# Kernel optimization log

Hardware: AMD Instinct MI355X
Metric: run time of the kernel (lower is better)

The kernel has to match this reference:

```python
import jax, jax.numpy as jnp
import numpy as np

N_NODES = 100000
N_EDGES = 1600000
C_IN = 128
C_OUT = 128


def setup_inputs() -> dict:
    key = jax.random.key(0)
    k1, k2, k3, k4 = jax.random.split(key, 4)
    x = jax.random.normal(k1, (N_NODES, C_IN), dtype=jnp.float32)
    edge_index = jax.random.randint(k2, (2, N_EDGES), 0, N_NODES, dtype=jnp.int64)
    W = jax.random.normal(k3, (C_IN, C_OUT), dtype=jnp.float32) * (1.0 / np.sqrt(C_IN))
    b = jax.random.normal(k4, (C_OUT,), dtype=jnp.float32) * 0.01
    return {"x": x, "edge_index": edge_index, "W": W, "b": b}


def reference(x, edge_index, W, b):
    # EffSparseEdgeOnlyConv with aggr='add':
    #   x2  = lin2(x)
    #   deg = A @ ones         (per-destination-node edge count)
    #   out = A @ x2 - x2 * deg
    n = x.shape[0]
    dst = edge_index[0]  # COO row indices (aggregation target)
    src = edge_index[1]  # COO col indices (message source)
    x2 = x @ W + b  # [N, C_out]
    deg = jax.ops.segment_sum(
        jnp.ones((src.shape[0],), dtype=x.dtype), dst, num_segments=n
    )[:, None]  # [N, 1]
    agg = jax.ops.segment_sum(x2[src], dst, num_segments=n)  # [N, C_out]
    return agg - x2 * deg
```

## Files before the change

kernel.cpp:

```cpp
#include <hip/hip_runtime.h>


#define C_DIM 128
#define EPB 8192
#define MAXBK 1024

typedef __attribute__((ext_vector_type(8))) short bf16x8;
typedef __attribute__((ext_vector_type(4))) float f32x4;

__device__ __forceinline__ ushort f2b(float f) {
    uint u = __float_as_uint(f);
    u = (u + 0x7FFFu + ((u >> 16) & 1u)) >> 16;
    return (ushort)u;
}
__device__ __forceinline__ float b2f_lo(uint u) { return __uint_as_float(u << 16); }
__device__ __forceinline__ float b2f_hi(uint u) { return __uint_as_float(u & 0xFFFF0000u); }

__global__ __launch_bounds__(256) void gemm_mfma(const float* __restrict__ x,
                                                 const float* __restrict__ W,
                                                 float* __restrict__ x2f,
                                                 ushort* __restrict__ x2b,
                                                 int nrows) {
    __shared__ ushort Wt[128 * 128];
    const int tid = threadIdx.x;
    for (int i = tid; i < 4096; i += 256) {
        int k = i >> 5, n0 = (i & 31) * 4;
        float4 w = *(const float4*)(W + k * 128 + n0);
        float wv[4] = {w.x, w.y, w.z, w.w};
#pragma unroll
        for (int j = 0; j < 4; j++) {
            int n = n0 + j;
            Wt[(n * 128 + k) ^ ((n & 7) << 3)] = f2b(wv[j]);
        }
    }
    __syncthreads();

    const int wv_ = tid >> 6;
    const int lane = tid & 63;
    const int ln = lane & 15, kg = lane >> 4;
    const int row_base = blockIdx.x * 128 + wv_ * 32;

    f32x4 acc[2][8];
#pragma unroll
    for (int a = 0; a < 2; a++)
#pragma unroll
        for (int b = 0; b < 8; b++) acc[a][b] = (f32x4)(0.f);

#pragma unroll
    for (int step = 0; step < 4; step++) {
        const int k0 = step * 32 + kg * 8;
        bf16x8 bfr[8];
#pragma unroll
        for (int cf = 0; cf < 8; cf++) {
            int n = cf * 16 + ln;
            bfr[cf] = *(const bf16x8*)&Wt[(n * 128 + k0) ^ ((n & 7) << 3)];
        }
#pragma unroll
        for (int mf = 0; mf < 2; mf++) {
            int row = row_base + mf * 16 + ln;
            bf16x8 afr;
#pragma unroll
            for (int j = 0; j < 8; j++) afr[j] = 0;
            if (row < nrows) {
                const float4* ap = (const float4*)(x + (size_t)row * 128 + k0);
                float4 a0 = ap[0], a1 = ap[1];
                float av[8] = {a0.x, a0.y, a0.z, a0.w, a1.x, a1.y, a1.z, a1.w};
#pragma unroll
                for (int j = 0; j < 8; j++) afr[j] = (short)f2b(av[j]);
            }
#pragma unroll
            for (int cf = 0; cf < 8; cf++)
                acc[mf][cf] = __builtin_amdgcn_mfma_f32_16x16x32_bf16(afr, bfr[cf], acc[mf][cf], 0, 0, 0);
        }
    }

#pragma unroll
    for (int mf = 0; mf < 2; mf++) {
#pragma unroll
        for (int j = 0; j < 4; j++) {
            int row = row_base + mf * 16 + kg * 4 + j;
            if (row >= nrows) continue;
#pragma unroll
            for (int cf = 0; cf < 8; cf++) {
                float v = acc[mf][cf][j];
                int col = cf * 16 + ln;
                x2f[(size_t)row * 128 + col] = v;
                if (x2b) x2b[(size_t)row * 128 + col] = f2b(v);
            }
        }
    }
}

__global__ __launch_bounds__(256) void zero_ints(int* p, int n) {
    int i = blockIdx.x * 256 + threadIdx.x;
    if (i < n) p[i] = 0;
}

__global__ __launch_bounds__(256) void count_deg(const int* __restrict__ ei,
                                                 int* __restrict__ cnt, int ne, int nn) {
    int e = blockIdx.x * 256 + threadIdx.x;
    if (e >= ne) return;
    int dst = ei[e];
    if ((unsigned)dst < (unsigned)nn) atomicAdd(&cnt[dst], 1);
}

__global__ __launch_bounds__(256) void scan_partials(const int* __restrict__ cnt,
                                                     int* __restrict__ bsum, int n) {
    __shared__ int red[256];
    int i = blockIdx.x * 1024 + threadIdx.x * 4;
    int s = 0;
    if (i + 3 < n) {
        int4 v = *(const int4*)(cnt + i);
        s = v.x + v.y + v.z + v.w;
    } else {
        for (int j = i; j < n && j < i + 4; j++) s += cnt[j];
    }
    red[threadIdx.x] = s;
    __syncthreads();
    for (int off = 128; off > 0; off >>= 1) {
        if (threadIdx.x < off) red[threadIdx.x] += red[threadIdx.x + off];
        __syncthreads();
    }
    if (threadIdx.x == 0) bsum[blockIdx.x] = red[0];
}

__global__ __launch_bounds__(1024) void scan_bsums(int* __restrict__ bsum, int nb) {
    __shared__ int s[1024];
    int v = (threadIdx.x < nb) ? bsum[threadIdx.x] : 0;
    s[threadIdx.x] = v;
    __syncthreads();
    for (int off = 1; off < 1024; off <<= 1) {
        int t = (threadIdx.x >= off) ? s[threadIdx.x - off] : 0;
        __syncthreads();
        s[threadIdx.x] += t;
        __syncthreads();
    }
    if (threadIdx.x < nb) bsum[threadIdx.x] = s[threadIdx.x] - v;
}

__global__ __launch_bounds__(256) void scan_apply(const int* __restrict__ cnt,
                                                  const int* __restrict__ bsum,
                                                  int* __restrict__ start, int n) {
    __shared__ int s[256];
    int i = blockIdx.x * 1024 + threadIdx.x * 4;
    int4 v = make_int4(0, 0, 0, 0);
    if (i + 3 < n) {
        v = *(const int4*)(cnt + i);
    } else {
        if (i + 0 < n) v.x = cnt[i + 0];
        if (i + 1 < n) v.y = cnt[i + 1];
        if (i + 2 < n) v.z = cnt[i + 2];
        if (i + 3 < n) v.w = cnt[i + 3];
    }
    int tsum = v.x + v.y + v.z + v.w;
    s[threadIdx.x] = tsum;
    __syncthreads();
    for (int off = 1; off < 256; off <<= 1) {
        int t = (threadIdx.x >= off) ? s[threadIdx.x - off] : 0;
        __syncthreads();
        s[threadIdx.x] += t;
        __syncthreads();
    }
    int r0 = s[threadIdx.x] - tsum + bsum[blockIdx.x];
    int r1 = r0 + v.x, r2 = r1 + v.y, r3 = r2 + v.z;
    if (i + 3 < n) {
        *(int4*)(start + i) = make_int4(r0, r1, r2, r3);
    } else {
        int rr[4] = {r0, r1, r2, r3};
        for (int j = 0; j < 4 && i + j < n; j++) start[i + j] = rr[j];
    }
}

__global__ __launch_bounds__(256) void bin_edges2(const int* __restrict__ ei,
                                                  const int* __restrict__ start,
                                                  int* __restrict__ bnext,
                                                  uint* __restrict__ bbuf,
                                                  int ne, int nn, int nbk) {
    __shared__ int hist[MAXBK];
    __shared__ int base[MAXBK];
    const int e0 = blockIdx.x * EPB;
    const int e1 = min(ne, e0 + EPB);
    for (int i = threadIdx.x; i < nbk; i += 256) hist[i] = 0;
    __syncthreads();
    for (int e = e0 + threadIdx.x; e < e1; e += 256) {
        int dst = ei[e];
        if ((unsigned)dst < (unsigned)nn) atomicAdd(&hist[dst >> 7], 1);
    }
    __syncthreads();
    for (int i = threadIdx.x; i < nbk; i += 256) {
        int h = hist[i];
        int b0 = (h > 0) ? atomicAdd(&bnext[i], h) : 0;
        base[i] = start[i << 7] + b0;
        hist[i] = 0;
    }
    __syncthreads();
    for (int e = e0 + threadIdx.x; e < e1; e += 256) {
        int dst = ei[e];
        int src = ei[ne + e];
        if ((unsigned)dst >= (unsigned)nn || (unsigned)src >= (unsigned)nn) continue;
        int b = dst >> 7;
        int r = atomicAdd(&hist[b], 1);
        bbuf[base[b] + r] = ((uint)(dst & 127) << 17) | (uint)src;
    }
}

__global__ __launch_bounds__(256) void sort_bucket(const uint* __restrict__ bbuf,
                                                   const int* __restrict__ start,
                                                   const int* __restrict__ cnt,
                                                   int* __restrict__ csr, int n) {
    __shared__ int lnext[128];
    __shared__ int sstart[128];
    const int b = blockIdx.x;
    const int d0 = b << 7;
    const int dlim = min(n, d0 + 128);
    if (threadIdx.x < 128) {
        lnext[threadIdx.x] = 0;
        sstart[threadIdx.x] = (d0 + threadIdx.x < n) ? start[d0 + threadIdx.x] : 0;
    }
    __syncthreads();
    const int base = sstart[0];
    const int last = dlim - 1 - d0;
    const int end = sstart[last] + cnt[d0 + last];
    for (int i = base + threadIdx.x; i < end; i += 256) {
        uint p = bbuf[i];
        int d7 = (int)(p >> 17);
        int src = (int)(p & 0x1FFFFu);
        int r = atomicAdd(&lnext[d7], 1);
        csr[sstart[d7] + r] = src;
    }
}

__global__ __launch_bounds__(256) void fill_csr(const int* __restrict__ ei,
                                                int* __restrict__ next,
                                                int* __restrict__ csr, int ne, int nn) {
    int e = blockIdx.x * 256 + threadIdx.x;
    if (e >= ne) return;
    int dst = ei[e];
    int src = ei[ne + e];
    if ((unsigned)dst >= (unsigned)nn || (unsigned)src >= (unsigned)nn) return;
    int slot = atomicAdd(&next[dst], 1);
    csr[slot] = src;
}
__global__ __launch_bounds__(256) void copy_ints(const int* __restrict__ a,
                                                 int* __restrict__ b, int n) {
    int i = blockIdx.x * 256 + threadIdx.x;
    if (i < n) b[i] = a[i];
}

__global__ __launch_bounds__(256) void gather_b16(const int* __restrict__ csr,
                                                  const int* __restrict__ start,
                                                  const int* __restrict__ cnt,
                                                  const uint* __restrict__ x2b,
                                                  const float* __restrict__ x2f,
                                                  float* __restrict__ out, int nn) {
    int wave = (int)((blockIdx.x * 256 + threadIdx.x) >> 6);
    int lane = threadIdx.x & 63;
    if (wave >= nn) return;
    const int s0 = start[wave];
    const int dg = cnt[wave];
    float a0 = 0, a1 = 0, b0 = 0, b1 = 0, c0 = 0, c1 = 0, d0 = 0, d1 = 0;
    int e = 0;
    for (; e + 4 <= dg; e += 4) {
        int s1 = csr[s0 + e], s2 = csr[s0 + e + 1];
        int s3 = csr[s0 + e + 2], s4 = csr[s0 + e + 3];
        uint u1 = x2b[(size_t)s1 * 64 + lane];
        uint u2 = x2b[(size_t)s2 * 64 + lane];
        uint u3 = x2b[(size_t)s3 * 64 + lane];
        uint u4 = x2b[(size_t)s4 * 64 + lane];
        a0 += b2f_lo(u1); a1 += b2f_hi(u1);
        b0 += b2f_lo(u2); b1 += b2f_hi(u2);
        c0 += b2f_lo(u3); c1 += b2f_hi(u3);
        d0 += b2f_lo(u4); d1 += b2f_hi(u4);
    }
    for (; e < dg; e++) {
        int s1 = csr[s0 + e];
        uint u1 = x2b[(size_t)s1 * 64 + lane];
        a0 += b2f_lo(u1); a1 += b2f_hi(u1);
    }
    float2 self = ((const float2*)(x2f + (size_t)wave * 128))[lane];
    float d = (float)dg;
    float2 o;
    o.x = (a0 + b0) + (c0 + d0) - d * self.x;
    o.y = (a1 + b1) + (c1 + d1) - d * self.y;
    ((float2*)out)[(size_t)wave * 64 + lane] = o;
}

__global__ __launch_bounds__(256) void gather_out(const int* __restrict__ csr,
                                                  const int* __restrict__ start,
                                                  const int* __restrict__ cnt,
                                                  const float* __restrict__ x2,
                                                  float* __restrict__ out, int nn) {
    int wave = (int)((blockIdx.x * 256 + threadIdx.x) >> 6);
    int lane = threadIdx.x & 63;
    if (wave >= nn) return;
    const int s0 = start[wave];
    const int dg = cnt[wave];
    const float2* __restrict__ base = (const float2*)x2;
    float2 acc0 = make_float2(0.f, 0.f), acc1 = make_float2(0.f, 0.f);
    int e = 0;
    for (; e + 2 <= dg; e += 2) {
        int s1 = csr[s0 + e], s2 = csr[s0 + e + 1];
        float2 v1 = base[(size_t)s1 * 64 + lane];
        float2 v2 = base[(size_t)s2 * 64 + lane];
        acc0.x += v1.x; acc0.y += v1.y;
        acc1.x += v2.x; acc1.y += v2.y;
    }
    if (e < dg) {
        int s1 = csr[s0 + e];
        float2 v1 = base[(size_t)s1 * 64 + lane];
        acc0.x += v1.x; acc0.y += v1.y;
    }
    float2 self = base[(size_t)wave * 64 + lane];
    float d = (float)dg;
    float2 o;
    o.x = acc0.x + acc1.x - d * self.x;
    o.y = acc0.y + acc1.y - d * self.y;
    ((float2*)out)[(size_t)wave * 64 + lane] = o;
}

extern "C" void kernel_launch(void* const* d_in, const int* in_sizes, int n_in,
                              void* d_out, int out_size, void* d_ws, size_t ws_size,
                              hipStream_t stream) {
    const float* x = (const float*)d_in[0];
    const int* ei = (const int*)d_in[1];
    const float* W = (const float*)d_in[2];
    float* out = (float*)d_out;

    const int n = in_sizes[0] / C_DIM;
    const int ne = in_sizes[1] / 2;
    const int nb = (n + 1023) / 1024;
    const int nbk = (n + 127) / 128;

    const size_t sz_x2f = (size_t)n * C_DIM * sizeof(float);
    const size_t sz_x2b = (size_t)n * C_DIM * sizeof(ushort);
    const size_t sz_int = (size_t)n * sizeof(int);
    const size_t sz_bs = (size_t)((nb + 3) & ~3) * sizeof(int);
    const size_t sz_bn = (size_t)((nbk + 3) & ~3) * sizeof(int);
    const size_t sz_e = (size_t)ne * sizeof(int);
    const size_t need_bin = sz_x2f + sz_x2b + 2 * sz_int + sz_bs + sz_bn + 2 * sz_e;
    const size_t need_b16 = sz_x2f + sz_x2b + 3 * sz_int + sz_bs + sz_e;
    const bool use_bin = ws_size >= need_bin && nbk <= MAXBK && n < (1 << 17);
    const bool use_b16 = use_bin || ws_size >= need_b16;

    char* ws = (char*)d_ws;
    float* x2f = (float*)ws;                ws += sz_x2f;
    ushort* x2b = nullptr;
    if (use_b16) { x2b = (ushort*)ws;       ws += sz_x2b; }
    int* cnt = (int*)ws;                    ws += sz_int;
    int* start = (int*)ws;                  ws += sz_int;
    int* bsum = (int*)ws;                   ws += sz_bs;
    int *bnext = nullptr, *csr = nullptr, *next = nullptr;
    uint* bbuf = nullptr;
    if (use_bin) {
        bnext = (int*)ws;                   ws += sz_bn;
        csr = (int*)ws;                     ws += sz_e;
        bbuf = (uint*)ws;
    } else {
        next = (int*)ws;                    ws += sz_int;
        csr = (int*)ws;
    }

    zero_ints<<<(n + 255) / 256, 256, 0, stream>>>(cnt, n);
    if (use_bin) zero_ints<<<(nbk + 255) / 256, 256, 0, stream>>>(bnext, nbk);

    int ntiles = (n + 127) / 128;
    gemm_mfma<<<ntiles, 256, 0, stream>>>(x, W, x2f, x2b, n);

    int eblocks = (ne + 255) / 256;
    count_deg<<<eblocks, 256, 0, stream>>>(ei, cnt, ne, n);

    scan_partials<<<nb, 256, 0, stream>>>(cnt, bsum, n);
    scan_bsums<<<1, 1024, 0, stream>>>(bsum, nb);
    scan_apply<<<nb, 256, 0, stream>>>(cnt, bsum, start, n);

    if (use_bin) {
        int binblocks = (ne + EPB - 1) / EPB;
        bin_edges2<<<binblocks, 256, 0, stream>>>(ei, start, bnext, bbuf, ne, n, nbk);
        sort_bucket<<<nbk, 256, 0, stream>>>(bbuf, start, cnt, csr, n);
    } else {
        copy_ints<<<(n + 255) / 256, 256, 0, stream>>>(start, next, n);
        fill_csr<<<eblocks, 256, 0, stream>>>(ei, next, csr, ne, n);
    }

    int gblocks = (n + 3) / 4;
    if (use_b16)
        gather_b16<<<gblocks, 256, 0, stream>>>(csr, start, cnt, (const uint*)x2b, x2f, out, n);
    else
        gather_out<<<gblocks, 256, 0, stream>>>(csr, start, cnt, x2f, out, n);
}
```

Measured before the change: 337.3 us.

## Derive per-node degree and CSR offsets inside bucket sort, drop global atomic count

The binned path no longer runs a global per-node atomic degree count and a three-kernel prefix scan. It builds a per-bucket histogram with shared-memory atomics, scans the bucket counts in a single block, and has each bucket-sort block compute per-node counts and start offsets locally before scattering into CSR. The fallback path folds the start-to-next copy into the scan kernel. The intent is to remove scattered global atomics and several small launches, at the cost of an extra pass over the destination indices in bucket_hist.

Result: faster. 280.4 us (-16.9%).

```diff
diff --git a/kernel.cpp b/kernel.cpp
--- a/kernel.cpp
+++ b/kernel.cpp
@@ -96,6 +96,121 @@
     if (i < n) p[i] = 0;
 }
 
+__global__ __launch_bounds__(256) void bucket_hist(const int* __restrict__ ei,
+                                                   int* __restrict__ bcnt,
+                                                   int ne, int nn, int nbk) {
+    __shared__ int hist[MAXBK];
+    const int e0 = blockIdx.x * EPB;
+    const int e1 = min(ne, e0 + EPB);
+    for (int i = threadIdx.x; i < nbk; i += 256) hist[i] = 0;
+    __syncthreads();
+    for (int e = e0 + threadIdx.x; e < e1; e += 256) {
+        int dst = ei[e];
+        if ((unsigned)dst < (unsigned)nn) atomicAdd(&hist[dst >> 7], 1);
+    }
+    __syncthreads();
+    for (int i = threadIdx.x; i < nbk; i += 256) {
+        int h = hist[i];
+        if (h > 0) atomicAdd(&bcnt[i], h);
+    }
+}
+
+__global__ __launch_bounds__(1024) void bucket_scan(const int* __restrict__ bcnt,
+                                                    int* __restrict__ bstart,
+                                                    int* __restrict__ bnext, int nbk) {
+    __shared__ int s[1024];
+    int v = (threadIdx.x < nbk) ? bcnt[threadIdx.x] : 0;
+    s[threadIdx.x] = v;
+    __syncthreads();
+    for (int off = 1; off < 1024; off <<= 1) {
+        int t = (threadIdx.x >= off) ? s[threadIdx.x - off] : 0;
+        __syncthreads();
+        s[threadIdx.x] += t;
+        __syncthreads();
+    }
+    if (threadIdx.x < nbk) {
+        bstart[threadIdx.x] = s[threadIdx.x] - v;
+        bnext[threadIdx.x] = 0;
+        if (threadIdx.x == nbk - 1) bstart[nbk] = s[threadIdx.x];
+    }
+}
+
+__global__ __launch_bounds__(256) void bin_edges2(const int* __restrict__ ei,
+                                                  const int* __restrict__ bstart,
+                                                  int* __restrict__ bnext,
+                                                  uint* __restrict__ bbuf,
+                                                  int ne, int nn, int nbk) {
+    __shared__ int hist[MAXBK];
+    __shared__ int base[MAXBK];
+    const int e0 = blockIdx.x * EPB;
+    const int e1 = min(ne, e0 + EPB);
+    for (int i = threadIdx.x; i < nbk; i += 256) hist[i] = 0;
+    __syncthreads();
+    for (int e = e0 + threadIdx.x; e < e1; e += 256) {
+        int dst = ei[e];
+        if ((unsigned)dst < (unsigned)nn) atomicAdd(&hist[dst >> 7], 1);
+    }
+    __syncthreads();
+    for (int i = threadIdx.x; i < nbk; i += 256) {
+        int h = hist[i];
+        int b0 = (h > 0) ? atomicAdd(&bnext[i], h) : 0;
+        base[i] = bstart[i] + b0;
+        hist[i] = 0;
+    }
+    __syncthreads();
+    for (int e = e0 + threadIdx.x; e < e1; e += 256) {
+        int dst = ei[e];
+        int src = ei[ne + e];
+        if ((unsigned)dst >= (unsigned)nn || (unsigned)src >= (unsigned)nn) continue;
+        int b = dst >> 7;
+        int r = atomicAdd(&hist[b], 1);
+        bbuf[base[b] + r] = ((uint)(dst & 127) << 17) | (uint)src;
+    }
+}
+
+__global__ __launch_bounds__(256) void sort_bucket2(const uint* __restrict__ bbuf,
+                                                    const int* __restrict__ bstart,
+                                                    int* __restrict__ csr,
+                                                    int* __restrict__ start,
+                                                    int* __restrict__ cnt, int n) {
+    __shared__ int h[128];
+    __shared__ int sb[128];
+    const int b = blockIdx.x;
+    const int d0 = b << 7;
+    const int base = bstart[b];
+    const int end = bstart[b + 1];
+    if (threadIdx.x < 128) h[threadIdx.x] = 0;
+    __syncthreads();
+    for (int i = base + threadIdx.x; i < end; i += 256)
+        atomicAdd(&h[bbuf[i] >> 17], 1);
+    __syncthreads();
+    if (threadIdx.x < 128) sb[threadIdx.x] = h[threadIdx.x];
+    __syncthreads();
+    for (int off = 1; off < 128; off <<= 1) {
+        int t = 0;
+        if (threadIdx.x < 128 && threadIdx.x >= off) t = sb[threadIdx.x - off];
+        __syncthreads();
+        if (threadIdx.x < 128) sb[threadIdx.x] += t;
+        __syncthreads();
+    }
+    if (threadIdx.x < 128) {
+        int excl = sb[threadIdx.x] - h[threadIdx.x];
+        int gbase = base + excl;
+        sb[threadIdx.x] = gbase;
+        int d = d0 + threadIdx.x;
+        if (d < n) { start[d] = gbase; cnt[d] = h[threadIdx.x]; }
+        h[threadIdx.x] = 0;
+    }
+    __syncthreads();
+    for (int i = base + threadIdx.x; i < end; i += 256) {
+        uint p = bbuf[i];
+        int d7 = (int)(p >> 17);
+        int src = (int)(p & 0x1FFFFu);
+        int r = atomicAdd(&h[d7], 1);
+        csr[sb[d7] + r] = src;
+    }
+}
+
 __global__ __launch_bounds__(256) void count_deg(const int* __restrict__ ei,
                                                  int* __restrict__ cnt, int ne, int nn) {
     int e = blockIdx.x * 256 + threadIdx.x;
@@ -140,7 +255,8 @@
 
 __global__ __launch_bounds__(256) void scan_apply(const int* __restrict__ cnt,
                                                   const int* __restrict__ bsum,
-                                                  int* __restrict__ start, int n) {
+                                                  int* __restrict__ start,
+                                                  int* __restrict__ next, int n) {
     __shared__ int s[256];
     int i = blockIdx.x * 1024 + threadIdx.x * 4;
     int4 v = make_int4(0, 0, 0, 0);
@@ -165,68 +281,13 @@
     int r1 = r0 + v.x, r2 = r1 + v.y, r3 = r2 + v.z;
     if (i + 3 < n) {
         *(int4*)(start + i) = make_int4(r0, r1, r2, r3);
+        *(int4*)(next + i) = make_int4(r0, r1, r2, r3);
     } else {
         int rr[4] = {r0, r1, r2, r3};
-        for (int j = 0; j < 4 && i + j < n; j++) start[i + j] = rr[j];
-    }
-}
-
-__global__ __launch_bounds__(256) void bin_edges2(const int* __restrict__ ei,
-                                                  const int* __restrict__ start,
-                                                  int* __restrict__ bnext,
-                                                  uint* __restrict__ bbuf,
-                                                  int ne, int nn, int nbk) {
-    __shared__ int hist[MAXBK];
-    __shared__ int base[MAXBK];
-    const int e0 = blockIdx.x * EPB;
-    const int e1 = min(ne, e0 + EPB);
-    for (int i = threadIdx.x; i < nbk; i += 256) hist[i] = 0;
-    __syncthreads();
-    for (int e = e0 + threadIdx.x; e < e1; e += 256) {
-        int dst = ei[e];
-        if ((unsigned)dst < (unsigned)nn) atomicAdd(&hist[dst >> 7], 1);
-    }
-    __syncthreads();
-    for (int i = threadIdx.x; i < nbk; i += 256) {
-        int h = hist[i];
-        int b0 = (h > 0) ? atomicAdd(&bnext[i], h) : 0;
-        base[i] = start[i << 7] + b0;
-        hist[i] = 0;
-    }
-    __syncthreads();
-    for (int e = e0 + threadIdx.x; e < e1; e += 256) {
-        int dst = ei[e];
-        int src = ei[ne + e];
-        if ((unsigned)dst >= (unsigned)nn || (unsigned)src >= (unsigned)nn) continue;
-        int b = dst >> 7;
-        int r = atomicAdd(&hist[b], 1);
-        bbuf[base[b] + r] = ((uint)(dst & 127) << 17) | (uint)src;
-    }
-}
-
-__global__ __launch_bounds__(256) void sort_bucket(const uint* __restrict__ bbuf,
-                                                   const int* __restrict__ start,
-                                                   const int* __restrict__ cnt,
-                                                   int* __restrict__ csr, int n) {
-    __shared__ int lnext[128];
-    __shared__ int sstart[128];
-    const int b = blockIdx.x;
-    const int d0 = b << 7;
-    const int dlim = min(n, d0 + 128);
-    if (threadIdx.x < 128) {
-        lnext[threadIdx.x] = 0;
-        sstart[threadIdx.x] = (d0 + threadIdx.x < n) ? start[d0 + threadIdx.x] : 0;
-    }
-    __syncthreads();
-    const int base = sstart[0];
-    const int last = dlim - 1 - d0;
-    const int end = sstart[last] + cnt[d0 + last];
-    for (int i = base + threadIdx.x; i < end; i += 256) {
-        uint p = bbuf[i];
-        int d7 = (int)(p >> 17);
-        int src = (int)(p & 0x1FFFFu);
-        int r = atomicAdd(&lnext[d7], 1);
-        csr[sstart[d7] + r] = src;
+        for (int j = 0; j < 4 && i + j < n; j++) {
+            start[i + j] = rr[j];
+            next[i + j] = rr[j];
+        }
     }
 }
 
@@ -240,11 +301,6 @@
     if ((unsigned)dst >= (unsigned)nn || (unsigned)src >= (unsigned)nn) return;
     int slot = atomicAdd(&next[dst], 1);
     csr[slot] = src;
-}
-__global__ __launch_bounds__(256) void copy_ints(const int* __restrict__ a,
-                                                 int* __restrict__ b, int n) {
-    int i = blockIdx.x * 256 + threadIdx.x;
-    if (i < n) b[i] = a[i];
 }
 
 __global__ __launch_bounds__(256) void gather_b16(const int* __restrict__ csr,
@@ -328,16 +384,16 @@
 
     const int n = in_sizes[0] / C_DIM;
     const int ne = in_sizes[1] / 2;
+    const int nbk = (n + 127) / 128;
     const int nb = (n + 1023) / 1024;
-    const int nbk = (n + 127) / 128;
 
     const size_t sz_x2f = (size_t)n * C_DIM * sizeof(float);
     const size_t sz_x2b = (size_t)n * C_DIM * sizeof(ushort);
     const size_t sz_int = (size_t)n * sizeof(int);
+    const size_t sz_bkt = (size_t)((nbk + 4) & ~3) * sizeof(int);
+    const size_t sz_e = (size_t)ne * sizeof(int);
     const size_t sz_bs = (size_t)((nb + 3) & ~3) * sizeof(int);
-    const size_t sz_bn = (size_t)((nbk + 3) & ~3) * sizeof(int);
-    const size_t sz_e = (size_t)ne * sizeof(int);
-    const size_t need_bin = sz_x2f + sz_x2b + 2 * sz_int + sz_bs + sz_bn + 2 * sz_e;
+    const size_t need_bin = sz_x2f + sz_x2b + 2 * sz_int + 3 * sz_bkt + 2 * sz_e;
     const size_t need_b16 = sz_x2f + sz_x2b + 3 * sz_int + sz_bs + sz_e;
     const bool use_bin = ws_size >= need_bin && nbk <= MAXBK && n < (1 << 17);
     const bool use_b16 = use_bin || ws_size >= need_b16;
@@ -348,37 +404,42 @@
     if (use_b16) { x2b = (ushort*)ws;       ws += sz_x2b; }
     int* cnt = (int*)ws;                    ws += sz_int;
     int* start = (int*)ws;                  ws += sz_int;
-    int* bsum = (int*)ws;                   ws += sz_bs;
-    int *bnext = nullptr, *csr = nullptr, *next = nullptr;
+    int *csr = nullptr, *next = nullptr, *bsum = nullptr;
+    int *bcnt = nullptr, *bstart = nullptr, *bnext = nullptr;
     uint* bbuf = nullptr;
+
     if (use_bin) {
-        bnext = (int*)ws;                   ws += sz_bn;
+        bcnt = (int*)ws;                    ws += sz_bkt;
+        bstart = (int*)ws;                  ws += sz_bkt;
+        bnext = (int*)ws;                   ws += sz_bkt;
         csr = (int*)ws;                     ws += sz_e;
         bbuf = (uint*)ws;
     } else {
+        bsum = (int*)ws;                    ws += sz_bs;
         next = (int*)ws;                    ws += sz_int;
         csr = (int*)ws;
     }
 
-    zero_ints<<<(n + 255) / 256, 256, 0, stream>>>(cnt, n);
-    if (use_bin) zero_ints<<<(nbk + 255) / 256, 256, 0, stream>>>(bnext, nbk);
-
     int ntiles = (n + 127) / 128;
-    gemm_mfma<<<ntiles, 256, 0, stream>>>(x, W, x2f, x2b, n);
-
+    int binblocks = (ne + EPB - 1) / EPB;
     int eblocks = (ne + 255) / 256;
-    count_deg<<<eblocks, 256, 0, stream>>>(ei, cnt, ne, n);
-
-    scan_partials<<<nb, 256, 0, stream>>>(cnt, bsum, n);
-    scan_bsums<<<1, 1024, 0, stream>>>(bsum, nb);
-    scan_apply<<<nb, 256, 0, stream>>>(cnt, bsum, start, n);
 
     if (use_bin) {
-        int binblocks = (ne + EPB - 1) / EPB;
-        bin_edges2<<<binblocks, 256, 0, stream>>>(ei, start, bnext, bbuf, ne, n, nbk);
-        sort_bucket<<<nbk, 256, 0, stream>>>(bbuf, start, cnt, csr, n);
+        zero_ints<<<(nbk + 255) / 256, 256, 0, stream>>>(bcnt, nbk);
+
+        gemm_mfma<<<ntiles, 256, 0, stream>>>(x, W, x2f, x2b, n);
+
+        bucket_hist<<<binblocks, 256, 0, stream>>>(ei, bcnt, ne, n, nbk);
+        bucket_scan<<<1, 1024, 0, stream>>>(bcnt, bstart, bnext, nbk);
+        bin_edges2<<<binblocks, 256, 0, stream>>>(ei, bstart, bnext, bbuf, ne, n, nbk);
+        sort_bucket2<<<nbk, 256, 0, stream>>>(bbuf, bstart, csr, start, cnt, n);
     } else {
-        copy_ints<<<(n + 255) / 256, 256, 0, stream>>>(start, next, n);
+        zero_ints<<<(n + 255) / 256, 256, 0, stream>>>(cnt, n);
+        gemm_mfma<<<ntiles, 256, 0, stream>>>(x, W, x2f, x2b, n);
+        count_deg<<<eblocks, 256, 0, stream>>>(ei, cnt, ne, n);
+        scan_partials<<<nb, 256, 0, stream>>>(cnt, bsum, n);
+        scan_bsums<<<1, 1024, 0, stream>>>(bsum, nb);
+        scan_apply<<<nb, 256, 0, stream>>>(cnt, bsum, start, next, n);
         fill_csr<<<eblocks, 256, 0, stream>>>(ei, next, csr, ne, n);
     }
 
```
